# Kernel optimization log

Measured on AMD Instinct MI355X. Metric: run time of the kernel, lower is better.

## Reference

```python
import jax, jax.numpy as jnp
import numpy as np

HIDDEN = 512


def setup_inputs() -> dict:
    key = jax.random.key(0)
    ks = jax.random.split(key, 5)
    S, B, I, H = 256, 128, 1024, HIDDEN
    scale_ih = 1.0 / np.sqrt(H)
    return {
        "x": jax.random.normal(ks[0], (S, B, I), dtype=jnp.float32),
        "w_ih": jax.random.normal(ks[1], (4 * H, I), dtype=jnp.float32) * scale_ih,
        "w_hh": jax.random.normal(ks[2], (4 * H, H), dtype=jnp.float32) * scale_ih,
        "b_ih": jax.random.normal(ks[3], (4 * H,), dtype=jnp.float32) * scale_ih,
        "b_hh": jax.random.normal(ks[4], (4 * H,), dtype=jnp.float32) * scale_ih,
    }


def reference(x, w_ih, w_hh, b_ih, b_hh):
    # x: [S, B, I]. LSTMCell with PyTorch gate order (i, f, g, o).
    S, B, _ = x.shape
    H = HIDDEN
    bias = b_ih + b_hh  # fuse both biases

    def step(carry, xt):
        h, c = carry
        gates = xt @ w_ih.T + h @ w_hh.T + bias  # [B, 4H]
        i, f, g, o = jnp.split(gates, 4, axis=-1)
        i = jax.nn.sigmoid(i)
        f = jax.nn.sigmoid(f)
        g = jnp.tanh(g)
        o = jax.nn.sigmoid(o)
        c = f * c + i * g
        h = o * jnp.tanh(c)
        # original code's h[arange(B)] / c[arange(B)] is an identity gather: no-op
        return (h, c), None

    h0 = jnp.zeros((B, H), dtype=x.dtype)
    c0 = jnp.zeros((B, H), dtype=x.dtype)
    (h, c), _ = jax.lax.scan(step, (h0, c0), x)
    return h.sum()
```

## Files before the change

### kernel.cpp

```cpp
#include <hip/hip_runtime.h>

typedef __attribute__((ext_vector_type(8))) short short8;
typedef __attribute__((ext_vector_type(4))) float f32x4;

#define S_LEN 256
#define BATCH 128
#define IN_DIM 1024
#define HID 512
#define G4 2048

#define SENT 0xFFFFFFFFu

__device__ __forceinline__ unsigned short f32_bf16(float f) {
  unsigned int u = __float_as_uint(f);
  u = (u + 0x7FFFu + ((u >> 16) & 1u)) >> 16;
  return (unsigned short)u;
}
__device__ __forceinline__ float bf16_f32(unsigned short h) {
  return __uint_as_float(((unsigned int)h) << 16);
}
__device__ __forceinline__ float sigm(float x) { return 1.0f / (1.0f + __expf(-x)); }
__device__ __forceinline__ float tanh_fast(float x) {
  return 1.0f - 2.0f / (__expf(2.0f * x) + 1.0f);
}

__global__ void cvt_bf16(const float* __restrict__ src, unsigned short* __restrict__ dst, int n) {
  int i = (blockIdx.x * blockDim.x + threadIdx.x) * 4;
  if (i >= n) return;
  float4 v = *(const float4*)(src + i);
  ushort4 o;
  o.x = f32_bf16(v.x); o.y = f32_bf16(v.y); o.z = f32_bf16(v.z); o.w = f32_bf16(v.w);
  *(ushort4*)(dst + i) = o;
}

__global__ void init_all(const float* __restrict__ b_ih, const float* __restrict__ b_hh,
                         float* __restrict__ bias, uint4* __restrict__ hring4) {
  int i = blockIdx.x * blockDim.x + threadIdx.x;
  if (i < G4) bias[i] = b_ih[i] + b_hh[i];
  const int SLOT4 = BATCH * HID / 8;
  const int TOT4 = 257 * SLOT4;
  const uint4 z = make_uint4(0u, 0u, 0u, 0u);
  const uint4 sN = make_uint4(SENT, SENT, SENT, SENT);
  for (int k = i; k < TOT4; k += gridDim.x * blockDim.x)
    hring4[k] = (k < SLOT4) ? z : sN;
}

__device__ __forceinline__ void gl_lds16(const void* g, void* l) {
  __builtin_amdgcn_global_load_lds(
      (const __attribute__((address_space(1))) unsigned int*)g,
      (__attribute__((address_space(3))) unsigned int*)l, 16, 0, 0);
}

template <int C_F32>
__global__ __launch_bounds__(256) void gemm_bias(
    const unsigned short* __restrict__ A,
    const unsigned short* __restrict__ Bw,
    const float* __restrict__ bias,
    void* __restrict__ Cout) {
  __shared__ __align__(16) unsigned short As[128 * 32];
  __shared__ __align__(16) unsigned short Bs[128 * 32];
  const int tid = threadIdx.x;
  const int w = tid >> 6, l = tid & 63;
  const int wm = w & 1, wn = w >> 1;
  const int nt = blockIdx.x & 15, mt = blockIdx.x >> 4;

  f32x4 acc[4][4];
#pragma unroll
  for (int i = 0; i < 4; i++)
#pragma unroll
    for (int j = 0; j < 4; j++) acc[i][j] = f32x4{0.f, 0.f, 0.f, 0.f};

  for (int k0 = 0; k0 < 1024; k0 += 32) {
    __syncthreads();
#pragma unroll
    for (int jj = 0; jj < 2; jj++) {
      int cid = (w * 2 + jj) * 64 + l;
      int row = cid >> 2, kc = cid & 3;
      const unsigned short* ga = A + (size_t)(mt * 128 + row) * 1024 + k0 + kc * 8;
      gl_lds16(ga, As + (w * 2 + jj) * 512);
      const unsigned short* gb = Bw + (size_t)(nt * 128 + row) * 1024 + k0 + kc * 8;
      gl_lds16(gb, Bs + (w * 2 + jj) * 512);
    }
    __syncthreads();
    short8 a[4], b[4];
#pragma unroll
    for (int i = 0; i < 4; i++)
      a[i] = *(const short8*)&As[(wm * 64 + i * 16 + (l & 15)) * 32 + (l >> 4) * 8];
#pragma unroll
    for (int j = 0; j < 4; j++)
      b[j] = *(const short8*)&Bs[(wn * 64 + j * 16 + (l & 15)) * 32 + (l >> 4) * 8];
#pragma unroll
    for (int i = 0; i < 4; i++)
#pragma unroll
      for (int j = 0; j < 4; j++)
        acc[i][j] = __builtin_amdgcn_mfma_f32_16x16x32_bf16(a[i], b[j], acc[i][j], 0, 0, 0);
  }
#pragma unroll
  for (int j = 0; j < 4; j++) {
    int cg = nt * 128 + wn * 64 + j * 16 + (l & 15);
    float bv = bias[cg];
#pragma unroll
    for (int i = 0; i < 4; i++) {
      int rbase = mt * 128 + wm * 64 + i * 16 + (l >> 4) * 4;
#pragma unroll
      for (int r = 0; r < 4; r++) {
        float v = acc[i][j][r] + bv;
        if (C_F32)
          ((float*)Cout)[(size_t)(rbase + r) * 2048 + cg] = v;
        else
          ((unsigned short*)Cout)[(size_t)(rbase + r) * 2048 + cg] = f32_bf16(v);
      }
    }
  }
}

__global__ __launch_bounds__(256, 1) void lstm_rec(
    const unsigned short* __restrict__ whh,
    const void* __restrict__ gx,
    int gx_f32,
    unsigned* __restrict__ hring) {
  __shared__ __align__(16) unsigned short Hs[2][16][520];
  __shared__ __align__(16) float Gt[16][132];

  const int tid = threadIdx.x;
  const int w = tid >> 6, l = tid & 63;
  const int m = blockIdx.x & 7;
  const int s = blockIdx.x >> 3;

  short8 bw[16][2];
#pragma unroll
  for (int u = 0; u < 2; u++) {
    int n = (2 * w + u) * 16 + (l & 15);
    int jn = n >> 2, g = n & 3;
    int R = g * 512 + s * 32 + jn;
    const unsigned short* base = whh + (size_t)R * 512 + ((l >> 4) * 8);
#pragma unroll
    for (int kk = 0; kk < 16; kk++) bw[kk][u] = *(const short8*)(base + kk * 32);
  }

  const int b = l & 15;
  const int p = 4 * w + (l >> 4);
  const int gb = m * 16 + b;
  const int colg = s * 32 + 2 * p;
  float c0 = 0.f, c1 = 0.f;

  const float* gxf = (const float*)gx;
  const unsigned short* gxb = (const unsigned short*)gx;
  const int SLOTW = BATCH * HID / 2;
  const unsigned long long* hull = (const unsigned long long*)hring;
  const int SLOTQ = BATCH * HID / 4;

  const int skc = tid & 127;
  const int srow = tid >> 7;
  const bool selfst = (((tid >> 3) & 15) == s);

  unsigned long long v[8];
#pragma unroll
  for (int it = 0; it < 8; it++)
    v[it] = __hip_atomic_load(&hull[(size_t)(m * 16 + it * 2 + srow) * 128 + skc],
                              __ATOMIC_RELAXED, __HIP_MEMORY_SCOPE_AGENT);
  float2 pg[4];
  {
    size_t base0 = (size_t)gb * G4 + colg;
    if (gx_f32) {
#pragma unroll
      for (int g = 0; g < 4; g++) pg[g] = *(const float2*)(gxf + base0 + (size_t)g * 512);
    } else {
#pragma unroll
      for (int g = 0; g < 4; g++) {
        unsigned u = *(const unsigned*)(gxb + base0 + (size_t)g * 512);
        pg[g].x = bf16_f32((unsigned short)(u & 0xFFFFu));
        pg[g].y = bf16_f32((unsigned short)(u >> 16));
      }
    }
  }

  for (int t = 0; t < S_LEN; t++) {
    const int buf = t & 1;
    const unsigned long long* src = hull + (size_t)t * SLOTQ;

    if (!(selfst && t > 0)) {
      for (;;) {
        int bad = 0;
#pragma unroll
        for (int it = 0; it < 8; it++)
          bad |= (((unsigned)v[it] == SENT) | ((unsigned)(v[it] >> 32) == SENT)) << it;
        if (!bad) break;
#pragma unroll
        for (int it = 0; it < 8; it++)
          if ((bad >> it) & 1)
            v[it] = __hip_atomic_load(&src[(size_t)(m * 16 + it * 2 + srow) * 128 + skc],
                                      __ATOMIC_RELAXED, __HIP_MEMORY_SCOPE_AGENT);
      }
#pragma unroll
      for (int it = 0; it < 8; it++)
        *(unsigned long long*)&Hs[buf][it * 2 + srow][skc * 4] = v[it];
    }
    __syncthreads();

    unsigned long long vn[8];
    float2 pgn[4];
    if (t + 1 < S_LEN) {
      if (!selfst) {
        const unsigned long long* srcn = hull + (size_t)(t + 1) * SLOTQ;
#pragma unroll
        for (int it = 0; it < 8; it++)
          vn[it] = __hip_atomic_load(&srcn[(size_t)(m * 16 + it * 2 + srow) * 128 + skc],
                                     __ATOMIC_RELAXED, __HIP_MEMORY_SCOPE_AGENT);
      }
      size_t basen = (size_t)((t + 1) * BATCH + gb) * G4 + colg;
      if (gx_f32) {
#pragma unroll
        for (int g = 0; g < 4; g++) pgn[g] = *(const float2*)(gxf + basen + (size_t)g * 512);
      } else {
#pragma unroll
        for (int g = 0; g < 4; g++) {
          unsigned u = *(const unsigned*)(gxb + basen + (size_t)g * 512);
          pgn[g].x = bf16_f32((unsigned short)(u & 0xFFFFu));
          pgn[g].y = bf16_f32((unsigned short)(u >> 16));
        }
      }
    }

    f32x4 acc0 = f32x4{0.f, 0.f, 0.f, 0.f};
    f32x4 acc1 = f32x4{0.f, 0.f, 0.f, 0.f};
#pragma unroll
    for (int kk = 0; kk < 16; kk++) {
      short8 a = *(const short8*)&Hs[buf][l & 15][kk * 32 + (l >> 4) * 8];
      acc0 = __builtin_amdgcn_mfma_f32_16x16x32_bf16(a, bw[kk][0], acc0, 0, 0, 0);
      acc1 = __builtin_amdgcn_mfma_f32_16x16x32_bf16(a, bw[kk][1], acc1, 0, 0, 0);
    }

#pragma unroll
    for (int r = 0; r < 4; r++) {
      Gt[(l >> 4) * 4 + r][(2 * w + 0) * 16 + (l & 15)] = acc0[r];
      Gt[(l >> 4) * 4 + r][(2 * w + 1) * 16 + (l & 15)] = acc1[r];
    }

    float4 g0 = *(const float4*)&Gt[b][8 * p];
    float4 g1 = *(const float4*)&Gt[b][8 * p + 4];
    float i0 = sigm(g0.x + pg[0].x), f0 = sigm(g0.y + pg[1].x);
    float gg0 = tanh_fast(g0.z + pg[2].x), o0 = sigm(g0.w + pg[3].x);
    c0 = f0 * c0 + i0 * gg0;
    float h0 = o0 * tanh_fast(c0);
    float i1 = sigm(g1.x + pg[0].y), f1 = sigm(g1.y + pg[1].y);
    float gg1 = tanh_fast(g1.z + pg[2].y), o1 = sigm(g1.w + pg[3].y);
    c1 = f1 * c1 + i1 * gg1;
    float h1 = o1 * tanh_fast(c1);
    unsigned hp = (unsigned)f32_bf16(h0) | ((unsigned)f32_bf16(h1) << 16);

    __hip_atomic_store(&hring[(size_t)(t + 1) * SLOTW + gb * 256 + s * 16 + p], hp,
                       __ATOMIC_RELAXED, __HIP_MEMORY_SCOPE_AGENT);
    *(unsigned*)&Hs[buf ^ 1][b][colg] = hp;

#pragma unroll
    for (int it = 0; it < 8; it++) v[it] = vn[it];
#pragma unroll
    for (int g = 0; g < 4; g++) pg[g] = pgn[g];
  }
}

__global__ void reduce_sum(const unsigned short* __restrict__ h, float* __restrict__ out) {
  __shared__ float red[256];
  int tid = threadIdx.x;
  float s = 0.f;
  for (int i = tid * 8; i < BATCH * HID; i += 256 * 8) {
    uint4 v = *(const uint4*)(h + i);
    unsigned int q[4] = {v.x, v.y, v.z, v.w};
#pragma unroll
    for (int k = 0; k < 4; k++) {
      s += bf16_f32((unsigned short)(q[k] & 0xFFFFu));
      s += bf16_f32((unsigned short)(q[k] >> 16));
    }
  }
  red[tid] = s;
  __syncthreads();
  for (int off = 128; off > 0; off >>= 1) {
    if (tid < off) red[tid] += red[tid + off];
    __syncthreads();
  }
  if (tid == 0) out[0] = red[0];
}

extern "C" void kernel_launch(void* const* d_in, const int* in_sizes, int n_in,
                              void* d_out, int out_size, void* d_ws, size_t ws_size,
                              hipStream_t stream) {
  const float* x = (const float*)d_in[0];
  const float* w_ih = (const float*)d_in[1];
  const float* w_hh = (const float*)d_in[2];
  const float* b_ih = (const float*)d_in[3];
  const float* b_hh = (const float*)d_in[4];

  char* ws = (char*)d_ws;
  unsigned short* x_bf = (unsigned short*)(ws);
  unsigned short* wih_bf = (unsigned short*)(ws + 67108864);
  unsigned short* whh_bf = (unsigned short*)(ws + 71303168);
  float* bias = (float*)(ws + 73400320);
  unsigned* hring = (unsigned*)(ws + 73408512);
  void* gx = (void*)(ws + 107094016);

  const size_t need_f32 = 107094016ull + (size_t)S_LEN * BATCH * G4 * 4;
  int gx_f32 = (ws_size >= need_f32) ? 1 : 0;

  cvt_bf16<<<(33554432 / 4 + 255) / 256, 256, 0, stream>>>(x, x_bf, 33554432);
  cvt_bf16<<<(2097152 / 4 + 255) / 256, 256, 0, stream>>>(w_ih, wih_bf, 2097152);
  cvt_bf16<<<(1048576 / 4 + 255) / 256, 256, 0, stream>>>(w_hh, whh_bf, 1048576);
  init_all<<<256, 256, 0, stream>>>(b_ih, b_hh, bias, (uint4*)hring);

  if (gx_f32)
    gemm_bias<1><<<4096, 256, 0, stream>>>(x_bf, wih_bf, bias, gx);
  else
    gemm_bias<0><<<4096, 256, 0, stream>>>(x_bf, wih_bf, bias, gx);

  void* args[] = {(void*)&whh_bf, (void*)&gx, (void*)&gx_f32, (void*)&hring};
  hipLaunchCooperativeKernel((const void*)lstm_rec, dim3(128), dim3(256), args, 0, stream);

  reduce_sum<<<1, 256, 0, stream>>>((const unsigned short*)(hring + 256 * (BATCH * HID / 2)),
                                    (float*)d_out);
}
```

Measured before the change: 1.204 ms.

## Place each batch group's recurrence on one XCD to use local L2 sync

The recurrent kernel now launches 256 cooperative blocks. Each block reads its XCC_ID and takes a rank within that XCD, so the 16 blocks that exchange h for a batch group sit on the same XCD and share one L2. The h ring is split into per-group rings, and polling and stores become plain volatile accesses that stay in local L2, with an agent-scope load every 64 spins as an escape path. If the placement check fails, it falls back to the old agent-scope path. This also drops the bf16 gate-precompute fallback, so gx is always fp32.

```diff
diff --git a/kernel.cpp b/kernel.cpp
--- a/kernel.cpp
+++ b/kernel.cpp
@@ -11,6 +11,10 @@
 
 #define SENT 0xFFFFFFFFu
 
+#define SLOT_U 4096
+#define SLOT_Q 2048
+#define GR_U (257 * SLOT_U)
+
 __device__ __forceinline__ unsigned short f32_bf16(float f) {
   unsigned int u = __float_as_uint(f);
   u = (u + 0x7FFFu + ((u >> 16) & 1u)) >> 16;
@@ -22,6 +26,20 @@
 __device__ __forceinline__ float sigm(float x) { return 1.0f / (1.0f + __expf(-x)); }
 __device__ __forceinline__ float tanh_fast(float x) {
   return 1.0f - 2.0f / (__expf(2.0f * x) + 1.0f);
+}
+
+template <bool L2>
+__device__ __forceinline__ unsigned long long ld8(const unsigned long long* p) {
+  if (L2) return *(volatile const unsigned long long*)p;
+  return __hip_atomic_load(p, __ATOMIC_RELAXED, __HIP_MEMORY_SCOPE_AGENT);
+}
+__device__ __forceinline__ unsigned long long ld8_agent(const unsigned long long* p) {
+  return __hip_atomic_load(p, __ATOMIC_RELAXED, __HIP_MEMORY_SCOPE_AGENT);
+}
+template <bool L2>
+__device__ __forceinline__ void st4(unsigned* p, unsigned v) {
+  if (L2) *(volatile unsigned*)p = v;
+  else __hip_atomic_store(p, v, __ATOMIC_RELAXED, __HIP_MEMORY_SCOPE_AGENT);
 }
 
 __global__ void cvt_bf16(const float* __restrict__ src, unsigned short* __restrict__ dst, int n) {
@@ -34,15 +52,19 @@
 }
 
 __global__ void init_all(const float* __restrict__ b_ih, const float* __restrict__ b_hh,
-                         float* __restrict__ bias, uint4* __restrict__ hring4) {
+                         float* __restrict__ bias, unsigned* __restrict__ ctrl,
+                         uint4* __restrict__ hring4) {
   int i = blockIdx.x * blockDim.x + threadIdx.x;
   if (i < G4) bias[i] = b_ih[i] + b_hh[i];
-  const int SLOT4 = BATCH * HID / 8;
-  const int TOT4 = 257 * SLOT4;
+  if (i < 64) ctrl[i] = 0u;
+  const int SLOT4 = SLOT_U / 4;
+  const int TOT4 = 8 * 257 * SLOT4;
   const uint4 z = make_uint4(0u, 0u, 0u, 0u);
   const uint4 sN = make_uint4(SENT, SENT, SENT, SENT);
-  for (int k = i; k < TOT4; k += gridDim.x * blockDim.x)
-    hring4[k] = (k < SLOT4) ? z : sN;
+  for (int k = i; k < TOT4; k += gridDim.x * blockDim.x) {
+    int slot = (k / SLOT4) % 257;
+    hring4[k] = (slot == 0) ? z : sN;
+  }
 }
 
 __device__ __forceinline__ void gl_lds16(const void* g, void* l) {
@@ -51,12 +73,11 @@
       (__attribute__((address_space(3))) unsigned int*)l, 16, 0, 0);
 }
 
-template <int C_F32>
 __global__ __launch_bounds__(256) void gemm_bias(
     const unsigned short* __restrict__ A,
     const unsigned short* __restrict__ Bw,
     const float* __restrict__ bias,
-    void* __restrict__ Cout) {
+    float* __restrict__ Cout) {
   __shared__ __align__(16) unsigned short As[128 * 32];
   __shared__ __align__(16) unsigned short Bs[128 * 32];
   const int tid = threadIdx.x;
@@ -103,29 +124,20 @@
     for (int i = 0; i < 4; i++) {
       int rbase = mt * 128 + wm * 64 + i * 16 + (l >> 4) * 4;
 #pragma unroll
-      for (int r = 0; r < 4; r++) {
-        float v = acc[i][j][r] + bv;
-        if (C_F32)
-          ((float*)Cout)[(size_t)(rbase + r) * 2048 + cg] = v;
-        else
-          ((unsigned short*)Cout)[(size_t)(rbase + r) * 2048 + cg] = f32_bf16(v);
-      }
-    }
-  }
-}
-
-__global__ __launch_bounds__(256, 1) void lstm_rec(
+      for (int r = 0; r < 4; r++)
+        Cout[(size_t)(rbase + r) * 2048 + cg] = acc[i][j][r] + bv;
+    }
+  }
+}
+
+template <bool L2>
+__device__ __forceinline__ void lstm_core(
+    int m, int s, int tid,
     const unsigned short* __restrict__ whh,
-    const void* __restrict__ gx,
-    int gx_f32,
-    unsigned* __restrict__ hring) {
-  __shared__ __align__(16) unsigned short Hs[2][16][520];
-  __shared__ __align__(16) float Gt[16][132];
-
-  const int tid = threadIdx.x;
+    const float* __restrict__ gxf,
+    unsigned* __restrict__ hring,
+    unsigned short (*Hs)[16][520], float (*Gt)[132]) {
   const int w = tid >> 6, l = tid & 63;
-  const int m = blockIdx.x & 7;
-  const int s = blockIdx.x >> 3;
 
   short8 bw[16][2];
 #pragma unroll
@@ -144,53 +156,44 @@
   const int colg = s * 32 + 2 * p;
   float c0 = 0.f, c1 = 0.f;
 
-  const float* gxf = (const float*)gx;
-  const unsigned short* gxb = (const unsigned short*)gx;
-  const int SLOTW = BATCH * HID / 2;
-  const unsigned long long* hull = (const unsigned long long*)hring;
-  const int SLOTQ = BATCH * HID / 4;
+  unsigned* gring = hring + (size_t)m * GR_U;
+  const unsigned long long* gq = (const unsigned long long*)gring;
 
   const int skc = tid & 127;
   const int srow = tid >> 7;
-  const bool selfst = (((tid >> 3) & 15) == s);
+  const bool selfst = ((skc >> 3) == s);
 
   unsigned long long v[8];
 #pragma unroll
   for (int it = 0; it < 8; it++)
-    v[it] = __hip_atomic_load(&hull[(size_t)(m * 16 + it * 2 + srow) * 128 + skc],
-                              __ATOMIC_RELAXED, __HIP_MEMORY_SCOPE_AGENT);
+    v[it] = ld8<L2>(&gq[(size_t)(it * 2 + srow) * 128 + skc]);
   float2 pg[4];
   {
     size_t base0 = (size_t)gb * G4 + colg;
-    if (gx_f32) {
-#pragma unroll
-      for (int g = 0; g < 4; g++) pg[g] = *(const float2*)(gxf + base0 + (size_t)g * 512);
-    } else {
-#pragma unroll
-      for (int g = 0; g < 4; g++) {
-        unsigned u = *(const unsigned*)(gxb + base0 + (size_t)g * 512);
-        pg[g].x = bf16_f32((unsigned short)(u & 0xFFFFu));
-        pg[g].y = bf16_f32((unsigned short)(u >> 16));
-      }
-    }
+#pragma unroll
+    for (int g = 0; g < 4; g++) pg[g] = *(const float2*)(gxf + base0 + (size_t)g * 512);
   }
 
   for (int t = 0; t < S_LEN; t++) {
     const int buf = t & 1;
-    const unsigned long long* src = hull + (size_t)t * SLOTQ;
+    const unsigned long long* src = gq + (size_t)t * SLOT_Q;
 
     if (!(selfst && t > 0)) {
+      int spins = 0;
       for (;;) {
         int bad = 0;
 #pragma unroll
         for (int it = 0; it < 8; it++)
           bad |= (((unsigned)v[it] == SENT) | ((unsigned)(v[it] >> 32) == SENT)) << it;
         if (!bad) break;
+        ++spins;
+        bool esc = L2 && ((spins & 63) == 0);
 #pragma unroll
         for (int it = 0; it < 8; it++)
-          if ((bad >> it) & 1)
-            v[it] = __hip_atomic_load(&src[(size_t)(m * 16 + it * 2 + srow) * 128 + skc],
-                                      __ATOMIC_RELAXED, __HIP_MEMORY_SCOPE_AGENT);
+          if ((bad >> it) & 1) {
+            const unsigned long long* q = &src[(size_t)(it * 2 + srow) * 128 + skc];
+            v[it] = esc ? ld8_agent(q) : ld8<L2>(q);
+          }
       }
 #pragma unroll
       for (int it = 0; it < 8; it++)
@@ -202,24 +205,14 @@
     float2 pgn[4];
     if (t + 1 < S_LEN) {
       if (!selfst) {
-        const unsigned long long* srcn = hull + (size_t)(t + 1) * SLOTQ;
+        const unsigned long long* srcn = gq + (size_t)(t + 1) * SLOT_Q;
 #pragma unroll
         for (int it = 0; it < 8; it++)
-          vn[it] = __hip_atomic_load(&srcn[(size_t)(m * 16 + it * 2 + srow) * 128 + skc],
-                                     __ATOMIC_RELAXED, __HIP_MEMORY_SCOPE_AGENT);
+          vn[it] = ld8<L2>(&srcn[(size_t)(it * 2 + srow) * 128 + skc]);
       }
       size_t basen = (size_t)((t + 1) * BATCH + gb) * G4 + colg;
-      if (gx_f32) {
-#pragma unroll
-        for (int g = 0; g < 4; g++) pgn[g] = *(const float2*)(gxf + basen + (size_t)g * 512);
-      } else {
-#pragma unroll
-        for (int g = 0; g < 4; g++) {
-          unsigned u = *(const unsigned*)(gxb + basen + (size_t)g * 512);
-          pgn[g].x = bf16_f32((unsigned short)(u & 0xFFFFu));
-          pgn[g].y = bf16_f32((unsigned short)(u >> 16));
-        }
-      }
+#pragma unroll
+      for (int g = 0; g < 4; g++) pgn[g] = *(const float2*)(gxf + basen + (size_t)g * 512);
     }
 
     f32x4 acc0 = f32x4{0.f, 0.f, 0.f, 0.f};
@@ -230,7 +223,6 @@
       acc0 = __builtin_amdgcn_mfma_f32_16x16x32_bf16(a, bw[kk][0], acc0, 0, 0, 0);
       acc1 = __builtin_amdgcn_mfma_f32_16x16x32_bf16(a, bw[kk][1], acc1, 0, 0, 0);
     }
-
 #pragma unroll
     for (int r = 0; r < 4; r++) {
       Gt[(l >> 4) * 4 + r][(2 * w + 0) * 16 + (l & 15)] = acc0[r];
@@ -249,8 +241,7 @@
     float h1 = o1 * tanh_fast(c1);
     unsigned hp = (unsigned)f32_bf16(h0) | ((unsigned)f32_bf16(h1) << 16);
 
-    __hip_atomic_store(&hring[(size_t)(t + 1) * SLOTW + gb * 256 + s * 16 + p], hp,
-                       __ATOMIC_RELAXED, __HIP_MEMORY_SCOPE_AGENT);
+    st4<L2>(&gring[(size_t)(t + 1) * SLOT_U + b * 256 + s * 16 + p], hp);
     *(unsigned*)&Hs[buf ^ 1][b][colg] = hp;
 
 #pragma unroll
@@ -260,17 +251,53 @@
   }
 }
 
-__global__ void reduce_sum(const unsigned short* __restrict__ h, float* __restrict__ out) {
+__global__ __launch_bounds__(256, 1) void lstm_rec(
+    const unsigned short* __restrict__ whh,
+    const float* __restrict__ gx,
+    unsigned* __restrict__ hring,
+    unsigned* __restrict__ ctrl) {
+  __shared__ __align__(16) unsigned short Hs[2][16][520];
+  __shared__ __align__(16) float Gt[16][132];
+  __shared__ unsigned sh_xcd, sh_rank, sh_mode;
+
+  const int tid = threadIdx.x;
+  if (tid == 0) {
+    unsigned x;
+    asm("s_getreg_b32 %0, hwreg(HW_REG_XCC_ID)" : "=s"(x));
+    x &= 7u;
+    unsigned r = __hip_atomic_fetch_add(&ctrl[x], 1u, __ATOMIC_RELAXED,
+                                        __HIP_MEMORY_SCOPE_AGENT);
+    __hip_atomic_fetch_add(&ctrl[8], 1u, __ATOMIC_RELEASE, __HIP_MEMORY_SCOPE_AGENT);
+    while (__hip_atomic_load(&ctrl[8], __ATOMIC_ACQUIRE, __HIP_MEMORY_SCOPE_AGENT) <
+           gridDim.x) {}
+    unsigned ok = 1;
+#pragma unroll
+    for (int g = 0; g < 8; g++)
+      ok &= (__hip_atomic_load(&ctrl[g], __ATOMIC_RELAXED, __HIP_MEMORY_SCOPE_AGENT) >= 16u);
+    sh_xcd = x; sh_rank = r; sh_mode = ok;
+  }
+  __syncthreads();
+
+  if (sh_mode) {
+    if (sh_rank < 16)
+      lstm_core<true>((int)sh_xcd, (int)sh_rank, tid, whh, gx, hring, Hs, Gt);
+  } else {
+    if (blockIdx.x < 128)
+      lstm_core<false>((int)(blockIdx.x & 7), (int)(blockIdx.x >> 3), tid, whh, gx, hring,
+                       Hs, Gt);
+  }
+}
+
+__global__ void reduce_sum(const unsigned* __restrict__ hring, float* __restrict__ out) {
   __shared__ float red[256];
   int tid = threadIdx.x;
   float s = 0.f;
-  for (int i = tid * 8; i < BATCH * HID; i += 256 * 8) {
-    uint4 v = *(const uint4*)(h + i);
-    unsigned int q[4] = {v.x, v.y, v.z, v.w};
-#pragma unroll
-    for (int k = 0; k < 4; k++) {
-      s += bf16_f32((unsigned short)(q[k] & 0xFFFFu));
-      s += bf16_f32((unsigned short)(q[k] >> 16));
+  for (int g = 0; g < 8; g++) {
+    const unsigned* base = hring + (size_t)g * GR_U + (size_t)256 * SLOT_U;
+    for (int i = tid; i < SLOT_U; i += 256) {
+      unsigned q = base[i];
+      s += bf16_f32((unsigned short)(q & 0xFFFFu));
+      s += bf16_f32((unsigned short)(q >> 16));
     }
   }
   red[tid] = s;
@@ -296,25 +323,19 @@
   unsigned short* wih_bf = (unsigned short*)(ws + 67108864);
   unsigned short* whh_bf = (unsigned short*)(ws + 71303168);
   float* bias = (float*)(ws + 73400320);
-  unsigned* hring = (unsigned*)(ws + 73408512);
-  void* gx = (void*)(ws + 107094016);
-
-  const size_t need_f32 = 107094016ull + (size_t)S_LEN * BATCH * G4 * 4;
-  int gx_f32 = (ws_size >= need_f32) ? 1 : 0;
+  unsigned* ctrl = (unsigned*)(ws + 73408512);
+  unsigned* hring = (unsigned*)(ws + 73408768);
+  float* gx = (float*)(ws + 107094272);
 
   cvt_bf16<<<(33554432 / 4 + 255) / 256, 256, 0, stream>>>(x, x_bf, 33554432);
   cvt_bf16<<<(2097152 / 4 + 255) / 256, 256, 0, stream>>>(w_ih, wih_bf, 2097152);
   cvt_bf16<<<(1048576 / 4 + 255) / 256, 256, 0, stream>>>(w_hh, whh_bf, 1048576);
-  init_all<<<256, 256, 0, stream>>>(b_ih, b_hh, bias, (uint4*)hring);
-
-  if (gx_f32)
-    gemm_bias<1><<<4096, 256, 0, stream>>>(x_bf, wih_bf, bias, gx);
-  else
-    gemm_bias<0><<<4096, 256, 0, stream>>>(x_bf, wih_bf, bias, gx);
-
-  void* args[] = {(void*)&whh_bf, (void*)&gx, (void*)&gx_f32, (void*)&hring};
-  hipLaunchCooperativeKernel((const void*)lstm_rec, dim3(128), dim3(256), args, 0, stream);
-
-  reduce_sum<<<1, 256, 0, stream>>>((const unsigned short*)(hring + 256 * (BATCH * HID / 2)),
-                                    (float*)d_out);
-}
+  init_all<<<256, 256, 0, stream>>>(b_ih, b_hh, bias, ctrl, (uint4*)hring);
+
+  gemm_bias<<<4096, 256, 0, stream>>>(x_bf, wih_bf, bias, gx);
+
+  void* args[] = {(void*)&whh_bf, (void*)&gx, (void*)&hring, (void*)&ctrl};
+  hipLaunchCooperativeKernel((const void*)lstm_rec, dim3(256), dim3(256), args, 0, stream);
+
+  reduce_sum<<<1, 256, 0, stream>>>(hring, (float*)d_out);
+}
```

New measurement: 2.349 ms. +95.0%, slower.
